# Kernel optimization log

Measured on AMD Instinct MI355X. Metric: run time of the kernel, lower is better.

Reference implementation:

```python
import jax, jax.numpy as jnp
import numpy as np

HIDDEN = 64

def gcn_conv(x, W, b, src, dst, num_nodes):
    # GCNConv: out = D^{-1/2} (A + I) D^{-1/2} (x @ W) + b
    h = x @ W                                            # [N, F_out]
    ones = jnp.ones(src.shape[0], dtype=x.dtype)
    deg = jax.ops.segment_sum(ones, dst, num_segments=num_nodes) + 1.0  # +1 for self-loop
    dinv = jax.lax.rsqrt(deg)                             # deg^{-1/2}, deg >= 1 so safe
    norm = dinv[src] * dinv[dst]                          # [E]
    msgs = h[src] * norm[:, None]                         # [E, F_out]
    agg = jax.ops.segment_sum(msgs, dst, num_segments=num_nodes)
    # self-loop contribution: norm for (i,i) edge = dinv[i]^2
    out = agg + h * (dinv * dinv)[:, None] + b
    return out


def setup_inputs() -> dict:
    key = jax.random.key(0)
    k1, k2, k3, k4, k5 = jax.random.split(key, 5)
    N, F_in, F_out, E = 50000, 256, 128, 1600000
    x = jax.random.normal(k1, (N, F_in), dtype=jnp.float32)
    edge_index = jax.random.randint(k2, (2, E), 0, N, dtype=jnp.int64)
    W1 = jax.random.normal(k3, (F_in, HIDDEN), dtype=jnp.float32) * (1.0 / np.sqrt(F_in))
    b1 = jnp.zeros((HIDDEN,), dtype=jnp.float32)
    W2 = jax.random.normal(k4, (HIDDEN, F_out), dtype=jnp.float32) * (1.0 / np.sqrt(HIDDEN))
    b2 = jnp.zeros((F_out,), dtype=jnp.float32)
    return {"x": x, "edge_index": edge_index, "W1": W1, "b1": b1, "W2": W2, "b2": b2}


def reference(x, edge_index, W1, b1, W2, b2):
    num_nodes = x.shape[0]
    src, dst = edge_index[0], edge_index[1]
    h = gcn_conv(x, W1, b1, src, dst, num_nodes)
    h = jax.nn.relu(h)
    # dropout is identity in eval mode (training=False)
    out = gcn_conv(h, W2, b2, src, dst, num_nodes)
    return out
```

## Files before the change

kernel.cpp:

```cpp
#include <hip/hip_runtime.h>

#define FI 256
#define FH 64
#define FO 128
#define ASORT_CHUNK 2048

__device__ __forceinline__ ushort f2bf(float x) {
    unsigned b = __float_as_uint(x);
    b += 0x7fffu + ((b >> 16) & 1u);
    return (ushort)(b >> 16);
}
__device__ __forceinline__ float bf2f(ushort u) {
    return __uint_as_float(((unsigned)u) << 16);
}


__global__ void zero_i32(int* __restrict__ p, int n) {
    int i = blockIdx.x * 256 + threadIdx.x;
    if (i < n) p[i] = 0;
}

__global__ void deg_cnt_kernel(const int* __restrict__ dst, int* __restrict__ cnt, int E) {
    int base = blockIdx.x * 1024 + threadIdx.x;
    #pragma unroll
    for (int q = 0; q < 4; ++q) {
        int e = base + q * 256;
        if (e < E) atomicAdd(&cnt[dst[e]], 1);
    }
}

__global__ void dinv_kernel(const int* __restrict__ cnt, float* __restrict__ dinv, int N) {
    int i = blockIdx.x * 256 + threadIdx.x;
    if (i < N) dinv[i] = rsqrtf((float)cnt[i] + 1.0f);
}


__global__ __launch_bounds__(256) void hist_part_kernel(const int* __restrict__ dst,
                                                        int* __restrict__ bucket_cnt, int E) {
    __shared__ int lcnt[256];
    int t = threadIdx.x;
    int base = blockIdx.x * ASORT_CHUNK;
    lcnt[t] = 0;
    __syncthreads();
    #pragma unroll
    for (int j = 0; j < 8; ++j) {
        int e = base + j * 256 + t;
        if (e < E) atomicAdd(&lcnt[((unsigned)dst[e]) >> 8], 1);
    }
    __syncthreads();
    int v = lcnt[t];
    if (v > 0) atomicAdd(&bucket_cnt[t], v);
}

__global__ __launch_bounds__(256) void bucket_scan_kernel(const int* __restrict__ bucket_cnt,
                                                          int* __restrict__ bucket_base,
                                                          int* __restrict__ bucket_pos, int E) {
    __shared__ int sc[256];
    int t = threadIdx.x;
    int sum = bucket_cnt[t];
    sc[t] = sum;
    __syncthreads();
    for (int off = 1; off < 256; off <<= 1) {
        int u = (t >= off) ? sc[t - off] : 0;
        __syncthreads();
        sc[t] += u;
        __syncthreads();
    }
    int excl = sc[t] - sum;
    bucket_base[t] = excl;
    bucket_pos[t]  = excl;
    if (t == 255) bucket_base[256] = sc[255];
}

__global__ __launch_bounds__(256) void binA_kernel(const int* __restrict__ src,
                                                   const int* __restrict__ dst,
                                                   int* __restrict__ bucket_pos,
                                                   unsigned* __restrict__ binned, int E) {
    __shared__ int lcnt[256];
    __shared__ int lbase[256];
    __shared__ int gbase[256];
    __shared__ int sc[256];
    __shared__ unsigned sorted[ASORT_CHUNK];
    int t = threadIdx.x;
    int base = blockIdx.x * ASORT_CHUNK;
    lcnt[t] = 0;
    __syncthreads();
    unsigned pk[8];
    short bb[8];
    short mi[8];
    #pragma unroll
    for (int j = 0; j < 8; ++j) {
        int e = base + j * 256 + t;
        if (e < E) {
            unsigned s = (unsigned)src[e];
            unsigned d = (unsigned)dst[e];
            pk[j] = s | (d << 16);
            int b = (int)(d >> 8);
            bb[j] = (short)b;
            mi[j] = (short)atomicAdd(&lcnt[b], 1);
        } else {
            bb[j] = -1;
        }
    }
    __syncthreads();
    int v = lcnt[t];
    sc[t] = v;
    __syncthreads();
    #pragma unroll
    for (int off = 1; off < 256; off <<= 1) {
        int u = (t >= off) ? sc[t - off] : 0;
        __syncthreads();
        sc[t] += u;
        __syncthreads();
    }
    lbase[t] = sc[t] - v;
    if (v > 0) gbase[t] = atomicAdd(&bucket_pos[t], v);
    __syncthreads();
    #pragma unroll
    for (int j = 0; j < 8; ++j)
        if (bb[j] >= 0) sorted[lbase[(int)bb[j]] + (int)mi[j]] = pk[j];
    int tot = sc[255];
    __syncthreads();
    for (int i = t; i < tot; i += 256) {
        unsigned vv = sorted[i];
        int b = (int)(vv >> 24);
        binned[gbase[b] + (i - lbase[b])] = vv;
    }
}

__global__ __launch_bounds__(256) void binB_kernel(const int* __restrict__ bucket_base,
                                                   const unsigned* __restrict__ binned,
                                                   int* __restrict__ rec4,
                                                   int* __restrict__ row_start,
                                                   int* __restrict__ cnt,
                                                   float* __restrict__ dinv, int N) {
    __shared__ int lcnt[256];
    __shared__ int sc[256];
    __shared__ int lstart[256];
    __shared__ int loff[256];
    int t = threadIdx.x;
    int d0 = blockIdx.x << 8;
    int start = bucket_base[blockIdx.x];
    int end   = bucket_base[blockIdx.x + 1];
    lcnt[t] = 0;
    __syncthreads();
    for (int i = start + t; i < end; i += 256)
        atomicAdd(&lcnt[(binned[i] >> 16) & 0xffu], 1);
    __syncthreads();
    int v = lcnt[t];
    sc[t] = v;
    __syncthreads();
    for (int off = 1; off < 256; off <<= 1) {
        int u = (t >= off) ? sc[t - off] : 0;
        __syncthreads();
        sc[t] += u;
        __syncthreads();
    }
    int st = start + sc[t] - v;
    lstart[t] = st;
    loff[t] = 0;
    if (d0 + t < N) {
        row_start[d0 + t] = st;
        cnt[d0 + t] = v;
        dinv[d0 + t] = rsqrtf((float)v + 1.0f);
    }
    __syncthreads();
    int i = start + t;
    for (; i + 768 < end; i += 1024) {
        unsigned v0 = binned[i];
        unsigned v1 = binned[i + 256];
        unsigned v2 = binned[i + 512];
        unsigned v3 = binned[i + 768];
        int dA = (int)((v0 >> 16) & 0xffu); int kA = atomicAdd(&loff[dA], 1);
        rec4[lstart[dA] + kA] = (int)(v0 & 0xffffu);
        int dB = (int)((v1 >> 16) & 0xffu); int kB = atomicAdd(&loff[dB], 1);
        rec4[lstart[dB] + kB] = (int)(v1 & 0xffffu);
        int dC = (int)((v2 >> 16) & 0xffu); int kC = atomicAdd(&loff[dC], 1);
        rec4[lstart[dC] + kC] = (int)(v2 & 0xffffu);
        int dD = (int)((v3 >> 16) & 0xffu); int kD = atomicAdd(&loff[dD], 1);
        rec4[lstart[dD] + kD] = (int)(v3 & 0xffffu);
    }
    for (; i < end; i += 256) {
        unsigned v4 = binned[i];
        int d = (int)((v4 >> 16) & 0xffu);
        int k = atomicAdd(&loff[d], 1);
        rec4[lstart[d] + k] = (int)(v4 & 0xffffu);
    }
}


#define ACC8(hv, wt)                                                   \
    acc[0] = fmaf(__uint_as_float((hv).x << 16),         wt, acc[0]);  \
    acc[1] = fmaf(__uint_as_float((hv).x & 0xffff0000u), wt, acc[1]);  \
    acc[2] = fmaf(__uint_as_float((hv).y << 16),         wt, acc[2]);  \
    acc[3] = fmaf(__uint_as_float((hv).y & 0xffff0000u), wt, acc[3]);  \
    acc[4] = fmaf(__uint_as_float((hv).z << 16),         wt, acc[4]);  \
    acc[5] = fmaf(__uint_as_float((hv).z & 0xffff0000u), wt, acc[5]);  \
    acc[6] = fmaf(__uint_as_float((hv).w << 16),         wt, acc[6]);  \
    acc[7] = fmaf(__uint_as_float((hv).w & 0xffff0000u), wt, acc[7]);

__global__ void gather_relu_kernel(const int* __restrict__ rec4, const int* __restrict__ row_start,
                                   const int* __restrict__ cnt, const float* __restrict__ dinv,
                                   const float* __restrict__ b1, float* __restrict__ out, int N) {
    int node = blockIdx.x * 4 + (threadIdx.x >> 6);
    if (node >= N) return;
    int L = threadIdx.x & 63;
    int g = L >> 3;
    int q = L & 7;
    const ushort* hb = (const ushort*)out;
    int beg = row_start[node];
    int n   = cnt[node];
    float dvd = dinv[node];
    float acc[8] = {0.f, 0.f, 0.f, 0.f, 0.f, 0.f, 0.f, 0.f};
    for (int c0 = 0; c0 < n; c0 += 64) {
        int idx_l = c0 + L;
        int sreg = node;
        float wreg = 0.f;
        if (idx_l < n) {
            sreg = rec4[beg + idx_l];
            wreg = dinv[sreg] * dvd;
        }
        int m = n - c0; if (m > 64) m = 64;
        int umax = (m + 7) >> 3;
        #pragma unroll 2
        for (int u = 0; u < umax; ++u) {
            int lane = u * 8 + g;
            int sidx  = __shfl(sreg, lane, 64);
            float wt  = __shfl(wreg, lane, 64);
            uint4 hv = *(const uint4*)(hb + (size_t)sidx * 256 + 128 + q * 8);
            ACC8(hv, wt)
        }
    }
    #pragma unroll
    for (int off = 8; off < 64; off <<= 1)
        #pragma unroll
        for (int j = 0; j < 8; ++j)
            acc[j] += __shfl_xor(acc[j], off, 64);
    if (L < 8) {
        float dv2 = dvd * dvd;
        uint4 ho = *(const uint4*)(hb + (size_t)node * 256 + 128 + q * 8);
        float4 bl = *(const float4*)&b1[q * 8];
        float4 bh = *(const float4*)&b1[q * 8 + 4];
        float r0 = fmaxf(acc[0] + dv2 * __uint_as_float(ho.x << 16)         + bl.x, 0.f);
        float r1 = fmaxf(acc[1] + dv2 * __uint_as_float(ho.x & 0xffff0000u) + bl.y, 0.f);
        float r2 = fmaxf(acc[2] + dv2 * __uint_as_float(ho.y << 16)         + bl.z, 0.f);
        float r3 = fmaxf(acc[3] + dv2 * __uint_as_float(ho.y & 0xffff0000u) + bl.w, 0.f);
        float r4 = fmaxf(acc[4] + dv2 * __uint_as_float(ho.z << 16)         + bh.x, 0.f);
        float r5 = fmaxf(acc[5] + dv2 * __uint_as_float(ho.z & 0xffff0000u) + bh.y, 0.f);
        float r6 = fmaxf(acc[6] + dv2 * __uint_as_float(ho.w << 16)         + bh.z, 0.f);
        float r7 = fmaxf(acc[7] + dv2 * __uint_as_float(ho.w & 0xffff0000u) + bh.w, 0.f);
        uint4 st;
        st.x = (unsigned)f2bf(r0) | ((unsigned)f2bf(r1) << 16);
        st.y = (unsigned)f2bf(r2) | ((unsigned)f2bf(r3) << 16);
        st.z = (unsigned)f2bf(r4) | ((unsigned)f2bf(r5) << 16);
        st.w = (unsigned)f2bf(r6) | ((unsigned)f2bf(r7) << 16);
        *(uint4*)((ushort*)out + (size_t)node * 256 + 192 + q * 8) = st;
    }
}

__global__ void gather_comb_kernel(const int* __restrict__ rec4, const int* __restrict__ row_start,
                                   const int* __restrict__ cnt, const float* __restrict__ dinv,
                                   float* __restrict__ out, int N) {
    int node = blockIdx.x * 4 + (threadIdx.x >> 6);
    if (node >= N) return;
    int L = threadIdx.x & 63;
    int g = L >> 3;
    int q = L & 7;
    const ushort* hb = (const ushort*)out;
    int beg = row_start[node];
    int n   = cnt[node];
    float dvd = dinv[node];
    float acc[8] = {0.f, 0.f, 0.f, 0.f, 0.f, 0.f, 0.f, 0.f};
    for (int c0 = 0; c0 < n; c0 += 64) {
        int idx_l = c0 + L;
        int sreg = node;
        float wreg = 0.f;
        if (idx_l < n) {
            sreg = rec4[beg + idx_l];
            wreg = dinv[sreg] * dvd;
        }
        int m = n - c0; if (m > 64) m = 64;
        int umax = (m + 7) >> 3;
        #pragma unroll 2
        for (int u = 0; u < umax; ++u) {
            int lane = u * 8 + g;
            int sidx  = __shfl(sreg, lane, 64);
            float wt  = __shfl(wreg, lane, 64);
            uint4 hv = *(const uint4*)(hb + (size_t)sidx * 256 + 192 + q * 8);
            ACC8(hv, wt)
        }
    }
    #pragma unroll
    for (int off = 8; off < 64; off <<= 1)
        #pragma unroll
        for (int j = 0; j < 8; ++j)
            acc[j] += __shfl_xor(acc[j], off, 64);
    if (L < 8) {
        float dv2 = dvd * dvd;
        uint4 ho = *(const uint4*)(hb + (size_t)node * 256 + 192 + q * 8);
        float4 o0, o1;
        o0.x = acc[0] + dv2 * __uint_as_float(ho.x << 16);
        o0.y = acc[1] + dv2 * __uint_as_float(ho.x & 0xffff0000u);
        o0.z = acc[2] + dv2 * __uint_as_float(ho.y << 16);
        o0.w = acc[3] + dv2 * __uint_as_float(ho.y & 0xffff0000u);
        o1.x = acc[4] + dv2 * __uint_as_float(ho.z << 16);
        o1.y = acc[5] + dv2 * __uint_as_float(ho.z & 0xffff0000u);
        o1.z = acc[6] + dv2 * __uint_as_float(ho.w << 16);
        o1.w = acc[7] + dv2 * __uint_as_float(ho.w & 0xffff0000u);
        *(float4*)&out[(size_t)node * FO + q * 8]     = o0;
        *(float4*)&out[(size_t)node * FO + q * 8 + 4] = o1;
    }
}


__global__ __launch_bounds__(256) void mm1_tiled(const float* __restrict__ x,
                                                 const float* __restrict__ W1,
                                                 float* __restrict__ out, int N) {
    __shared__ float xs[32][128];
    __shared__ float ws[32][64];
    int tid = threadIdx.x;
    int R0  = blockIdx.x * 128;
    int ty  = tid >> 3;
    int tx  = tid & 7;
    float acc[4][8];
    #pragma unroll
    for (int i = 0; i < 4; ++i)
        #pragma unroll
        for (int j = 0; j < 8; ++j) acc[i][j] = 0.f;

    int sr = tid >> 1;
    int sk = (tid & 1) * 16;
    bool row_ok = (R0 + sr) < N;
    const float* xrow = x + (size_t)(R0 + sr) * FI;

    for (int k0 = 0; k0 < FI; k0 += 32) {
        __syncthreads();
        #pragma unroll
        for (int q = 0; q < 4; ++q) {
            float4 v = row_ok ? *(const float4*)&xrow[k0 + sk + q * 4]
                              : make_float4(0.f, 0.f, 0.f, 0.f);
            xs[sk + q * 4 + 0][sr] = v.x;
            xs[sk + q * 4 + 1][sr] = v.y;
            xs[sk + q * 4 + 2][sr] = v.z;
            xs[sk + q * 4 + 3][sr] = v.w;
        }
        {
            int f = tid * 2;
            *(float4*)&ws[0][0 + f * 4]     = *(const float4*)&W1[(size_t)k0 * 64 + f * 4];
            *(float4*)&ws[0][0 + f * 4 + 4] = *(const float4*)&W1[(size_t)k0 * 64 + f * 4 + 4];
        }
        __syncthreads();
        #pragma unroll 4
        for (int k = 0; k < 32; ++k) {
            float4 a  = *(const float4*)&xs[k][ty * 4];
            float4 bl = *(const float4*)&ws[k][tx * 4];
            float4 bh = *(const float4*)&ws[k][32 + tx * 4];
            float av[4] = {a.x, a.y, a.z, a.w};
            float bv[8] = {bl.x, bl.y, bl.z, bl.w, bh.x, bh.y, bh.z, bh.w};
            #pragma unroll
            for (int i = 0; i < 4; ++i)
                #pragma unroll
                for (int j = 0; j < 8; ++j)
                    acc[i][j] = fmaf(av[i], bv[j], acc[i][j]);
        }
    }
    #pragma unroll
    for (int i = 0; i < 4; ++i) {
        int row = R0 + ty * 4 + i;
        if (row < N) {
            ushort* ob = (ushort*)out + (size_t)row * 256 + 128;
            ushort4 lo = {f2bf(acc[i][0]), f2bf(acc[i][1]), f2bf(acc[i][2]), f2bf(acc[i][3])};
            ushort4 hi = {f2bf(acc[i][4]), f2bf(acc[i][5]), f2bf(acc[i][6]), f2bf(acc[i][7])};
            *(ushort4*)&ob[tx * 4]      = lo;
            *(ushort4*)&ob[32 + tx * 4] = hi;
        }
    }
}

__global__ __launch_bounds__(256) void mm2_tiled(const float* __restrict__ W2,
                                                 const float* __restrict__ b2,
                                                 float* __restrict__ out, int N) {
    __shared__ float xs[64][68];
    __shared__ float ws[64][128];
    int tid = threadIdx.x;
    int R0  = blockIdx.x * 64;
    int ty  = tid >> 4;
    int tx  = tid & 15;

    {
        int sr = tid >> 2;
        int l4 = tid & 3;
        int grow = R0 + sr;
        bool ok = grow < N;
        const float* orow = out + (size_t)grow * FO;
        #pragma unroll
        for (int q = 0; q < 4; ++q) {
            int j0 = (l4 + 4 * q) * 4;
            float4 a = ok ? *(const float4*)&orow[j0] : make_float4(0.f, 0.f, 0.f, 0.f);
            xs[j0 + 0][sr] = a.x;
            xs[j0 + 1][sr] = a.y;
            xs[j0 + 2][sr] = a.z;
            xs[j0 + 3][sr] = a.w;
        }
    }
    #pragma unroll
    for (int q = 0; q < 8; ++q) {
        int f = tid + q * 256;
        *(float4*)&ws[f >> 5][(f & 31) * 4] = *(const float4*)&W2[(size_t)f * 4];
    }
    __syncthreads();

    float acc[4][8];
    #pragma unroll
    for (int i = 0; i < 4; ++i)
        #pragma unroll
        for (int j = 0; j < 8; ++j) acc[i][j] = 0.f;

    #pragma unroll 4
    for (int k = 0; k < FH; ++k) {
        float4 a  = *(const float4*)&xs[k][ty * 4];
        float4 bl = *(const float4*)&ws[k][tx * 4];
        float4 bh = *(const float4*)&ws[k][64 + tx * 4];
        float av[4] = {a.x, a.y, a.z, a.w};
        float bv[8] = {bl.x, bl.y, bl.z, bl.w, bh.x, bh.y, bh.z, bh.w};
        #pragma unroll
        for (int i = 0; i < 4; ++i)
            #pragma unroll
            for (int j = 0; j < 8; ++j)
                acc[i][j] = fmaf(av[i], bv[j], acc[i][j]);
    }

    float4 b2l = *(const float4*)&b2[tx * 4];
    float4 b2h = *(const float4*)&b2[64 + tx * 4];
    #pragma unroll
    for (int i = 0; i < 4; ++i) {
        int row = R0 + ty * 4 + i;
        if (row < N) {
            float* o = out + (size_t)row * FO;
            *(float4*)&o[tx * 4] = make_float4(acc[i][0] + b2l.x, acc[i][1] + b2l.y,
                                               acc[i][2] + b2l.z, acc[i][3] + b2l.w);
            *(float4*)&o[64 + tx * 4] = make_float4(acc[i][4] + b2h.x, acc[i][5] + b2h.y,
                                                    acc[i][6] + b2h.z, acc[i][7] + b2h.w);
        }
    }
}


__global__ void expand_hs1_kernel(float* __restrict__ out, int N) {
    int row = blockIdx.x * 4 + (threadIdx.x >> 6);
    if (row >= N) return;
    int lane = threadIdx.x & 63;
    float v = bf2f(((const ushort*)out)[(size_t)row * 256 + 128 + lane]);
    out[(size_t)row * FO + FH + lane] = v;
}

__global__ void zero_half_kernel(float* __restrict__ out, int half, int N) {
    int i = blockIdx.x * 256 + threadIdx.x;
    if (i >= N * FH) return;
    out[(size_t)(i >> 6) * FO + half + (i & 63)] = 0.f;
}

__global__ void scatter_half_kernel(const int* __restrict__ src, const int* __restrict__ dst,
                                    const float* __restrict__ dinv, float* __restrict__ out,
                                    int rh, int wh, int E) {
    int e = blockIdx.x * 4 + (threadIdx.x >> 6);
    if (e >= E) return;
    int lane = threadIdx.x & 63;
    int s = src[e];
    int d = dst[e];
    float w = dinv[s] * dinv[d];
    atomicAdd(&out[(size_t)d * FO + wh + lane], out[(size_t)s * FO + rh + lane] * w);
}

__global__ void finish1_kernel(float* __restrict__ out, const float* __restrict__ dinv,
                               const float* __restrict__ b1, int N) {
    int i = blockIdx.x * 256 + threadIdx.x;
    if (i >= N * FH) return;
    int row = i >> 6;
    int c   = i & 63;
    size_t base = (size_t)row * FO;
    float dv = dinv[row];
    out[base + c] = fmaxf(out[base + c] + dv * dv * out[base + FH + c] + b1[c], 0.f);
}

__global__ void finish2_kernel(float* __restrict__ out, const float* __restrict__ dinv, int N) {
    int i = blockIdx.x * 256 + threadIdx.x;
    if (i >= N * FH) return;
    int row = i >> 6;
    int c   = i & 63;
    size_t base = (size_t)row * FO;
    float dv = dinv[row];
    out[base + c] = out[base + FH + c] + dv * dv * out[base + c];
}

extern "C" void kernel_launch(void* const* d_in, const int* in_sizes, int n_in,
                              void* d_out, int out_size, void* d_ws, size_t ws_size,
                              hipStream_t stream) {
    const float* x  = (const float*)d_in[0];
    const int*   ei = (const int*)d_in[1];
    const float* W1 = (const float*)d_in[2];
    const float* b1 = (const float*)d_in[3];
    const float* W2 = (const float*)d_in[4];
    const float* b2 = (const float*)d_in[5];
    float* out = (float*)d_out;

    int N = in_sizes[0] / FI;
    int E = in_sizes[1] / 2;
    const int* src = ei;
    const int* dst = ei + E;

    char* w = (char*)d_ws;
    float* dinv        = (float*)w;      w += (size_t)N * 4;
    int*   cnt         = (int*)w;        w += (size_t)N * 4;
    int*   row_start   = (int*)w;        w += (size_t)N * 4;
    int*   bucket_cnt  = (int*)w;        w += 256 * 4;
    int*   bucket_pos  = (int*)w;        w += 256 * 4;
    int*   bucket_base = (int*)w;        w += 260 * 4;
    unsigned* binned   = (unsigned*)w;   w += (size_t)E * 4;
    int*   rec4        = (int*)w;        w += (size_t)E * 4;
    size_t need = (size_t)(w - (char*)d_ws);

    int nblkA = (E + ASORT_CHUNK - 1) / ASORT_CHUNK;
    int nbk   = (N + 255) >> 8;

    if (ws_size >= need && N <= 65536) {
        zero_i32<<<1, 256, 0, stream>>>(bucket_cnt, 256);
        hist_part_kernel<<<nblkA, 256, 0, stream>>>(dst, bucket_cnt, E);
        bucket_scan_kernel<<<1, 256, 0, stream>>>(bucket_cnt, bucket_base, bucket_pos, E);
        binA_kernel<<<nblkA, 256, 0, stream>>>(src, dst, bucket_pos, binned, E);
        binB_kernel<<<nbk, 256, 0, stream>>>(bucket_base, binned, rec4, row_start, cnt, dinv, N);

        mm1_tiled<<<(N + 127) / 128, 256, 0, stream>>>(x, W1, out, N);
        gather_relu_kernel<<<(N + 3) / 4, 256, 0, stream>>>(rec4, row_start, cnt, dinv, b1, out, N);
        gather_comb_kernel<<<(N + 3) / 4, 256, 0, stream>>>(rec4, row_start, cnt, dinv, out, N);
        mm2_tiled<<<(N + 63) / 64, 256, 0, stream>>>(W2, b2, out, N);
    } else {
        zero_i32<<<(N + 255) / 256, 256, 0, stream>>>(cnt, N);
        deg_cnt_kernel<<<(E + 1023) / 1024, 256, 0, stream>>>(dst, cnt, E);
        dinv_kernel<<<(N + 255) / 256, 256, 0, stream>>>(cnt, dinv, N);
        mm1_tiled<<<(N + 127) / 128, 256, 0, stream>>>(x, W1, out, N);
        expand_hs1_kernel<<<(N + 3) / 4, 256, 0, stream>>>(out, N);
        zero_half_kernel<<<((N * FH) + 255) / 256, 256, 0, stream>>>(out, 0, N);
        scatter_half_kernel<<<(E + 3) / 4, 256, 0, stream>>>(src, dst, dinv, out, FH, 0, E);
        finish1_kernel<<<((N * FH) + 255) / 256, 256, 0, stream>>>(out, dinv, b1, N);
        zero_half_kernel<<<((N * FH) + 255) / 256, 256, 0, stream>>>(out, FH, N);
        scatter_half_kernel<<<(E + 3) / 4, 256, 0, stream>>>(src, dst, dinv, out, 0, FH, E);
        finish2_kernel<<<((N * FH) + 255) / 256, 256, 0, stream>>>(out, dinv, N);
        mm2_tiled<<<(N + 63) / 64, 256, 0, stream>>>(W2, b2, out, N);
    }
}
```

Baseline: 275.8 us.

## Batch gather loads ahead of FMAs and register-prefetch a larger mm1 tile

The two gather kernels now issue all up-to-8 neighbour row loads per 64-edge chunk before doing any FMAs, so more memory requests are in flight per wave. mm1 now runs 128 threads per block, each computing an 8x8 output tile. The next 32-wide K slice of x and W1 is prefetched into registers while the current slice is consumed from shared memory, and results are written with a single 16-byte store. The costs are higher register pressure in both kernels and fewer threads per block in mm1, which may lower occupancy.

```diff
diff --git a/kernel.cpp b/kernel.cpp
--- a/kernel.cpp
+++ b/kernel.cpp
@@ -199,6 +199,34 @@
     acc[6] = fmaf(__uint_as_float((hv).w << 16),         wt, acc[6]);  \
     acc[7] = fmaf(__uint_as_float((hv).w & 0xffff0000u), wt, acc[7]);
 
+#define GATHER_CHUNK(OFFS)                                                     \
+    for (int c0 = 0; c0 < n; c0 += 64) {                                       \
+        int idx_l = c0 + L;                                                    \
+        int sreg = node;                                                       \
+        float wreg = 0.f;                                                      \
+        if (idx_l < n) {                                                       \
+            sreg = rec4[beg + idx_l];                                          \
+            wreg = dinv[sreg] * dvd;                                           \
+        }                                                                      \
+        int m = n - c0; if (m > 64) m = 64;                                    \
+        int umax = (m + 7) >> 3;                                               \
+        uint4 hv[8];                                                           \
+        _Pragma("unroll")                                                      \
+        for (int u = 0; u < 8; ++u) {                                          \
+            if (u < umax) {                                                    \
+                int sidx = __shfl(sreg, u * 8 + g, 64);                        \
+                hv[u] = *(const uint4*)(hb + (size_t)sidx * 256 + (OFFS) + q * 8); \
+            }                                                                  \
+        }                                                                      \
+        _Pragma("unroll")                                                      \
+        for (int u = 0; u < 8; ++u) {                                          \
+            if (u < umax) {                                                    \
+                float wt = __shfl(wreg, u * 8 + g, 64);                        \
+                ACC8(hv[u], wt)                                                \
+            }                                                                  \
+        }                                                                      \
+    }
+
 __global__ void gather_relu_kernel(const int* __restrict__ rec4, const int* __restrict__ row_start,
                                    const int* __restrict__ cnt, const float* __restrict__ dinv,
                                    const float* __restrict__ b1, float* __restrict__ out, int N) {
@@ -212,25 +240,7 @@
     int n   = cnt[node];
     float dvd = dinv[node];
     float acc[8] = {0.f, 0.f, 0.f, 0.f, 0.f, 0.f, 0.f, 0.f};
-    for (int c0 = 0; c0 < n; c0 += 64) {
-        int idx_l = c0 + L;
-        int sreg = node;
-        float wreg = 0.f;
-        if (idx_l < n) {
-            sreg = rec4[beg + idx_l];
-            wreg = dinv[sreg] * dvd;
-        }
-        int m = n - c0; if (m > 64) m = 64;
-        int umax = (m + 7) >> 3;
-        #pragma unroll 2
-        for (int u = 0; u < umax; ++u) {
-            int lane = u * 8 + g;
-            int sidx  = __shfl(sreg, lane, 64);
-            float wt  = __shfl(wreg, lane, 64);
-            uint4 hv = *(const uint4*)(hb + (size_t)sidx * 256 + 128 + q * 8);
-            ACC8(hv, wt)
-        }
-    }
+    GATHER_CHUNK(128)
     #pragma unroll
     for (int off = 8; off < 64; off <<= 1)
         #pragma unroll
@@ -271,25 +281,7 @@
     int n   = cnt[node];
     float dvd = dinv[node];
     float acc[8] = {0.f, 0.f, 0.f, 0.f, 0.f, 0.f, 0.f, 0.f};
-    for (int c0 = 0; c0 < n; c0 += 64) {
-        int idx_l = c0 + L;
-        int sreg = node;
-        float wreg = 0.f;
-        if (idx_l < n) {
-            sreg = rec4[beg + idx_l];
-            wreg = dinv[sreg] * dvd;
-        }
-        int m = n - c0; if (m > 64) m = 64;
-        int umax = (m + 7) >> 3;
-        #pragma unroll 2
-        for (int u = 0; u < umax; ++u) {
-            int lane = u * 8 + g;
-            int sidx  = __shfl(sreg, lane, 64);
-            float wt  = __shfl(wreg, lane, 64);
-            uint4 hv = *(const uint4*)(hb + (size_t)sidx * 256 + 192 + q * 8);
-            ACC8(hv, wt)
-        }
-    }
+    GATHER_CHUNK(192)
     #pragma unroll
     for (int off = 8; off < 64; off <<= 1)
         #pragma unroll
@@ -313,7 +305,7 @@
 }
 
 
-__global__ __launch_bounds__(256) void mm1_tiled(const float* __restrict__ x,
+__global__ __launch_bounds__(128) void mm1_tiled(const float* __restrict__ x,
                                                  const float* __restrict__ W1,
                                                  float* __restrict__ out, int N) {
     __shared__ float xs[32][128];
@@ -322,57 +314,76 @@
     int R0  = blockIdx.x * 128;
     int ty  = tid >> 3;
     int tx  = tid & 7;
-    float acc[4][8];
-    #pragma unroll
-    for (int i = 0; i < 4; ++i)
+    float acc[8][8];
+    #pragma unroll
+    for (int i = 0; i < 8; ++i)
         #pragma unroll
         for (int j = 0; j < 8; ++j) acc[i][j] = 0.f;
 
-    int sr = tid >> 1;
-    int sk = (tid & 1) * 16;
-    bool row_ok = (R0 + sr) < N;
-    const float* xrow = x + (size_t)(R0 + sr) * FI;
-
-    for (int k0 = 0; k0 < FI; k0 += 32) {
-        __syncthreads();
-        #pragma unroll
-        for (int q = 0; q < 4; ++q) {
-            float4 v = row_ok ? *(const float4*)&xrow[k0 + sk + q * 4]
-                              : make_float4(0.f, 0.f, 0.f, 0.f);
-            xs[sk + q * 4 + 0][sr] = v.x;
-            xs[sk + q * 4 + 1][sr] = v.y;
-            xs[sk + q * 4 + 2][sr] = v.z;
-            xs[sk + q * 4 + 3][sr] = v.w;
-        }
-        {
-            int f = tid * 2;
-            *(float4*)&ws[0][0 + f * 4]     = *(const float4*)&W1[(size_t)k0 * 64 + f * 4];
-            *(float4*)&ws[0][0 + f * 4 + 4] = *(const float4*)&W1[(size_t)k0 * 64 + f * 4 + 4];
-        }
-        __syncthreads();
-        #pragma unroll 4
+    int xrow = R0 + tid;
+    bool ok = xrow < N;
+    const float* xr = x + (size_t)xrow * FI;
+    const float4 z4 = make_float4(0.f, 0.f, 0.f, 0.f);
+
+    float4 xv[8], wv[4];
+    #pragma unroll
+    for (int i = 0; i < 8; ++i) xv[i] = ok ? *(const float4*)&xr[i * 4] : z4;
+    #pragma unroll
+    for (int i = 0; i < 4; ++i) {
+        int idx = tid * 4 + i;
+        wv[i] = *(const float4*)&W1[(size_t)(idx >> 4) * 64 + (idx & 15) * 4];
+    }
+
+    for (int t = 0; t < 8; ++t) {
+        __syncthreads();
+        #pragma unroll
+        for (int i = 0; i < 8; ++i) {
+            xs[i * 4 + 0][tid] = xv[i].x;
+            xs[i * 4 + 1][tid] = xv[i].y;
+            xs[i * 4 + 2][tid] = xv[i].z;
+            xs[i * 4 + 3][tid] = xv[i].w;
+        }
+        #pragma unroll
+        for (int i = 0; i < 4; ++i) {
+            int idx = tid * 4 + i;
+            *(float4*)&ws[idx >> 4][(idx & 15) * 4] = wv[i];
+        }
+        __syncthreads();
+        if (t < 7) {
+            int k0 = (t + 1) * 32;
+            #pragma unroll
+            for (int i = 0; i < 8; ++i) xv[i] = ok ? *(const float4*)&xr[k0 + i * 4] : z4;
+            #pragma unroll
+            for (int i = 0; i < 4; ++i) {
+                int idx = tid * 4 + i;
+                wv[i] = *(const float4*)&W1[(size_t)(k0 + (idx >> 4)) * 64 + (idx & 15) * 4];
+            }
+        }
+        #pragma unroll 8
         for (int k = 0; k < 32; ++k) {
-            float4 a  = *(const float4*)&xs[k][ty * 4];
-            float4 bl = *(const float4*)&ws[k][tx * 4];
-            float4 bh = *(const float4*)&ws[k][32 + tx * 4];
-            float av[4] = {a.x, a.y, a.z, a.w};
-            float bv[8] = {bl.x, bl.y, bl.z, bl.w, bh.x, bh.y, bh.z, bh.w};
+            float4 al = *(const float4*)&xs[k][ty * 8];
+            float4 ah = *(const float4*)&xs[k][ty * 8 + 4];
+            float4 bl = *(const float4*)&ws[k][tx * 8];
+            float4 bh = *(const float4*)&ws[k][tx * 8 + 4];
+            float a[8] = {al.x, al.y, al.z, al.w, ah.x, ah.y, ah.z, ah.w};
+            float b[8] = {bl.x, bl.y, bl.z, bl.w, bh.x, bh.y, bh.z, bh.w};
             #pragma unroll
-            for (int i = 0; i < 4; ++i)
+            for (int i = 0; i < 8; ++i)
                 #pragma unroll
                 for (int j = 0; j < 8; ++j)
-                    acc[i][j] = fmaf(av[i], bv[j], acc[i][j]);
-        }
-    }
-    #pragma unroll
-    for (int i = 0; i < 4; ++i) {
-        int row = R0 + ty * 4 + i;
+                    acc[i][j] = fmaf(a[i], b[j], acc[i][j]);
+        }
+    }
+    #pragma unroll
+    for (int i = 0; i < 8; ++i) {
+        int row = R0 + ty * 8 + i;
         if (row < N) {
-            ushort* ob = (ushort*)out + (size_t)row * 256 + 128;
-            ushort4 lo = {f2bf(acc[i][0]), f2bf(acc[i][1]), f2bf(acc[i][2]), f2bf(acc[i][3])};
-            ushort4 hi = {f2bf(acc[i][4]), f2bf(acc[i][5]), f2bf(acc[i][6]), f2bf(acc[i][7])};
-            *(ushort4*)&ob[tx * 4]      = lo;
-            *(ushort4*)&ob[32 + tx * 4] = hi;
+            uint4 st;
+            st.x = (unsigned)f2bf(acc[i][0]) | ((unsigned)f2bf(acc[i][1]) << 16);
+            st.y = (unsigned)f2bf(acc[i][2]) | ((unsigned)f2bf(acc[i][3]) << 16);
+            st.z = (unsigned)f2bf(acc[i][4]) | ((unsigned)f2bf(acc[i][5]) << 16);
+            st.w = (unsigned)f2bf(acc[i][6]) | ((unsigned)f2bf(acc[i][7]) << 16);
+            *(uint4*)((ushort*)out + (size_t)row * 256 + 128 + tx * 8) = st;
         }
     }
 }
@@ -530,7 +541,7 @@
         binA_kernel<<<nblkA, 256, 0, stream>>>(src, dst, bucket_pos, binned, E);
         binB_kernel<<<nbk, 256, 0, stream>>>(bucket_base, binned, rec4, row_start, cnt, dinv, N);
 
-        mm1_tiled<<<(N + 127) / 128, 256, 0, stream>>>(x, W1, out, N);
+        mm1_tiled<<<(N + 127) / 128, 128, 0, stream>>>(x, W1, out, N);
         gather_relu_kernel<<<(N + 3) / 4, 256, 0, stream>>>(rec4, row_start, cnt, dinv, b1, out, N);
         gather_comb_kernel<<<(N + 3) / 4, 256, 0, stream>>>(rec4, row_start, cnt, dinv, out, N);
         mm2_tiled<<<(N + 63) / 64, 256, 0, stream>>>(W2, b2, out, N);
@@ -538,7 +549,7 @@
         zero_i32<<<(N + 255) / 256, 256, 0, stream>>>(cnt, N);
         deg_cnt_kernel<<<(E + 1023) / 1024, 256, 0, stream>>>(dst, cnt, E);
         dinv_kernel<<<(N + 255) / 256, 256, 0, stream>>>(cnt, dinv, N);
-        mm1_tiled<<<(N + 127) / 128, 256, 0, stream>>>(x, W1, out, N);
+        mm1_tiled<<<(N + 127) / 128, 128, 0, stream>>>(x, W1, out, N);
         expand_hs1_kernel<<<(N + 3) / 4, 256, 0, stream>>>(out, N);
         zero_half_kernel<<<((N * FH) + 255) / 256, 256, 0, stream>>>(out, 0, N);
         scatter_half_kernel<<<(E + 3) / 4, 256, 0, stream>>>(src, dst, dinv, out, FH, 0, E);
```

Result: slower. 311.4 us (+12.9%).
